# Kernel tuning notes

Measured on AMD Instinct MI355X. Metric: run time of the kernel, lower is better.

## Reference

```python
import jax, jax.numpy as jnp
import numpy as np

B, N, D, H = 32, 2048, 1024, 16
HD = D // H


def setup_inputs() -> dict:
    key = jax.random.key(0)
    ks = jax.random.split(key, 12)
    s = 1.0 / np.sqrt(D)  # xavier-ish scale for square projections
    return {
        "z": jax.random.normal(ks[0], (B, N, D), dtype=jnp.float32),
        "mask": jax.random.bernoulli(ks[1], 0.9, (B, N)),
        "query": jax.random.normal(ks[2], (1, 1, D), dtype=jnp.float32) * s,
        "w_q": jax.random.normal(ks[3], (D, D), dtype=jnp.float32) * s,
        "w_k": jax.random.normal(ks[4], (D, D), dtype=jnp.float32) * s,
        "w_v": jax.random.normal(ks[5], (D, D), dtype=jnp.float32) * s,
        "b_q": jnp.zeros((D,), dtype=jnp.float32),
        "b_k": jnp.zeros((D,), dtype=jnp.float32),
        "b_v": jnp.zeros((D,), dtype=jnp.float32),
        "w_o": jax.random.normal(ks[6], (D, D), dtype=jnp.float32) * s,
        "b_o": jnp.zeros((D,), dtype=jnp.float32),
    }


def reference(z, mask, query, w_q, w_k, w_v, b_q, b_k, b_v, w_o, b_o):
    # mask: True = valid key. Guarantee at least one valid key per row
    # (torch code sets mask[b, 0] = True for all-False rows).
    all_false = ~jnp.any(mask, axis=1)                 # [B]
    valid = mask.at[:, 0].set(mask[:, 0] | all_false)  # [B, N]

    # Projections (PyTorch Linear: x @ W.T + b)
    q = (query @ w_q.T + b_q).reshape(H, HD)           # single shared query -> [H, HD]
    k = (z @ w_k.T + b_k).reshape(B, N, H, HD)
    v = (z @ w_v.T + b_v).reshape(B, N, H, HD)

    scale = 1.0 / jnp.sqrt(jnp.asarray(HD, dtype=z.dtype))
    scores = jnp.einsum('hd,bnhd->bhn', q, k) * scale  # [B, H, N]
    scores = jnp.where(valid[:, None, :], scores, -jnp.inf)
    attn = jax.nn.softmax(scores, axis=-1)             # [B, H, N]

    pooled = jnp.einsum('bhn,bnhd->bhd', attn, v).reshape(B, D)
    return pooled @ w_o.T + b_o                        # [B, D]
```

## Files before the change

kernel.cpp:

```cpp
#include <hip/hip_runtime.h>
#include <hip/hip_bf16.h>
#include <stdint.h>

#define B_ 32
#define N_ 2048
#define D_ 1024
#define H_ 16

#define NT 16
#define RPAD 1028

typedef __attribute__((ext_vector_type(8))) short short8;
typedef __attribute__((ext_vector_type(4))) float f32x4;

__device__ __forceinline__ unsigned short f2bf(float x) {
    unsigned u = __float_as_uint(x);
    u += 0x7FFFu + ((u >> 16) & 1u);
    return (unsigned short)(u >> 16);
}
__device__ __forceinline__ float bflo(unsigned u) { return __uint_as_float(u << 16); }

__device__ __forceinline__ short8 cvt8(float4 a, float4 b) {
    union { __hip_bfloat162 h[4]; short8 s; } u;
    u.h[0] = __float22bfloat162_rn(make_float2(a.x, a.y));
    u.h[1] = __float22bfloat162_rn(make_float2(a.z, a.w));
    u.h[2] = __float22bfloat162_rn(make_float2(b.x, b.y));
    u.h[3] = __float22bfloat162_rn(make_float2(b.z, b.w));
    return u.s;
}

__global__ __launch_bounds__(256) void prep_k(const float* __restrict__ query,
        const float* __restrict__ w_q, const float* __restrict__ b_q,
        const float* __restrict__ w_k, const int* __restrict__ mask,
        unsigned short* __restrict__ rAf, int* __restrict__ any_ws) {
    __shared__ __align__(16) float qv[1024];
    __shared__ float qp[64][5];
    __shared__ float qh[64];
    __shared__ int wf[4];
    int bx = blockIdx.x, t = threadIdx.x;
    if (bx < 64) {
        int h = bx >> 2, dg = bx & 3;
        *(float4*)&qv[4 * t] = *(const float4*)&query[4 * t];
        __syncthreads();
        {
            int j = t >> 2, sub = t & 3;
            const float4* wq4 = (const float4*)(w_q + (size_t)(h * 64 + j) * 1024);
            const float4* qv4 = (const float4*)qv;
            float a = 0.f;
            #pragma unroll 8
            for (int kk = 0; kk < 64; kk++) {
                float4 wv = wq4[sub * 64 + kk];
                float4 vv = qv4[sub * 64 + kk];
                a += wv.x * vv.x + wv.y * vv.y + wv.z * vv.z + wv.w * vv.w;
            }
            qp[j][sub] = a;
        }
        __syncthreads();
        if (t < 64)
            qh[t] = qp[t][0] + qp[t][1] + qp[t][2] + qp[t][3] + b_q[h * 64 + t];
        __syncthreads();
        int d = dg * 256 + t;
        float acc = 0.f;
        #pragma unroll 8
        for (int j = 0; j < 64; j++)
            acc += qh[j] * w_k[(size_t)(h * 64 + j) * 1024 + d];
        acc *= 0.125f;
        int i = d >> 5, fq = (d >> 3) & 3, jj = d & 7;
        int lane = (fq << 4) | h;
        rAf[(size_t)(i * 64 + lane) * 8 + jj] = f2bf(acc);
    } else {
        int b = bx - 64;
        int v = 0;
        for (int k = 0; k < 8; k++) v |= mask[b * N_ + k * 256 + t];
        unsigned long long bal = __ballot(v != 0);
        int w = t >> 6;
        if ((t & 63) == 0) wf[w] = (bal != 0ull) ? 1 : 0;
        __syncthreads();
        if (t == 0) any_ws[b] = wf[0] | wf[1] | wf[2] | wf[3];
    }
}

__global__ __launch_bounds__(512, 2) void main_k(const float* __restrict__ z,
        const int* __restrict__ mask, const int* __restrict__ any_ws,
        const unsigned short* __restrict__ rAf,
        unsigned short* __restrict__ part, float* __restrict__ l_part) {
    __shared__ __align__(16) float zt[2][16 * RPAD];
    __shared__ __align__(16) float Ew[8][16][16];
    __shared__ int mlds[256];
    int bx = blockIdx.x, t = threadIdx.x;
    int b = bx >> 3, c = bx & 7;
    int n0 = c * 256;
    int w = t >> 6, l = t & 63;
    int frow = l & 15, fquad = l >> 4;
    int anyb = any_ws[b];

    short8 rA[32];
    {
        const short8* rA8 = (const short8*)rAf;
        #pragma unroll
        for (int i = 0; i < 32; i++) rA[i] = rA8[i * 64 + l];
    }
    const float* zb = z + (size_t)b * N_ * D_ + (size_t)n0 * D_;

    if (t < 256) mlds[t] = mask[b * N_ + n0 + t];

    float2 ctx[16];
    #pragma unroll
    for (int h = 0; h < 16; h++) ctx[h] = make_float2(0.f, 0.f);
    float l4[4] = {0.f, 0.f, 0.f, 0.f};

    #define STAGE(p, tile)                                                        \
        {                                                                         \
            _Pragma("unroll")                                                     \
            for (int rr = 0; rr < 2; rr++) {                                      \
                int row = 2 * w + rr;                                             \
                const float* gsrc = zb + (size_t)(tile) * 16 * D_ +               \
                                    (size_t)row * D_ + l * 4;                     \
                float* ldst = &zt[(p)][row * RPAD];                               \
                _Pragma("unroll")                                                 \
                for (int q = 0; q < 4; q++) {                                     \
                    __builtin_amdgcn_global_load_lds(                             \
                        (const __attribute__((address_space(1))) unsigned int*)   \
                            (gsrc + q * 256),                                     \
                        (__attribute__((address_space(3))) unsigned int*)         \
                            (ldst + q * 256),                                     \
                        16, 0, 0);                                                \
                }                                                                 \
            }                                                                     \
        }

    STAGE(0, 0)
    __syncthreads();

    for (int it = 0; it < NT; it++) {
        int p = it & 1;
        if (it + 1 < NT) STAGE(p ^ 1, it + 1)

        f32x4 a0 = {0.f,0.f,0.f,0.f}, a1 = {0.f,0.f,0.f,0.f};
        f32x4 a2 = {0.f,0.f,0.f,0.f}, a3 = {0.f,0.f,0.f,0.f};
        const float* brow = &zt[p][frow * RPAD + fquad * 8];
        #pragma unroll
        for (int i = 0; i < 32; i += 4) {
            float4 z00 = *(const float4*)(brow + (i + 0) * 32);
            float4 z01 = *(const float4*)(brow + (i + 0) * 32 + 4);
            float4 z10 = *(const float4*)(brow + (i + 1) * 32);
            float4 z11 = *(const float4*)(brow + (i + 1) * 32 + 4);
            float4 z20 = *(const float4*)(brow + (i + 2) * 32);
            float4 z21 = *(const float4*)(brow + (i + 2) * 32 + 4);
            float4 z30 = *(const float4*)(brow + (i + 3) * 32);
            float4 z31 = *(const float4*)(brow + (i + 3) * 32 + 4);
            a0 = __builtin_amdgcn_mfma_f32_16x16x32_bf16(rA[i + 0], cvt8(z00, z01), a0, 0, 0, 0);
            a1 = __builtin_amdgcn_mfma_f32_16x16x32_bf16(rA[i + 1], cvt8(z10, z11), a1, 0, 0, 0);
            a2 = __builtin_amdgcn_mfma_f32_16x16x32_bf16(rA[i + 2], cvt8(z20, z21), a2, 0, 0, 0);
            a3 = __builtin_amdgcn_mfma_f32_16x16x32_bf16(rA[i + 3], cvt8(z30, z31), a3, 0, 0, 0);
        }
        f32x4 acc = a0 + a1 + a2 + a3;

        {
            int gn = n0 + it * 16 + frow;
            bool valid = (mlds[it * 16 + frow] != 0) || (gn == 0 && anyb == 0);
            float e0 = valid ? __expf(acc[0]) : 0.f;
            float e1 = valid ? __expf(acc[1]) : 0.f;
            float e2 = valid ? __expf(acc[2]) : 0.f;
            float e3 = valid ? __expf(acc[3]) : 0.f;
            l4[0] += e0; l4[1] += e1; l4[2] += e2; l4[3] += e3;
            *(float4*)&Ew[w][frow][fquad * 4] = make_float4(e0, e1, e2, e3);
        }

        {
            const float* zcol = &zt[p][w * 128 + 2 * l];
            #pragma unroll 4
            for (int r = 0; r < 16; r++) {
                float2 zr = *(const float2*)(zcol + r * RPAD);
                const float4* er4 = (const float4*)&Ew[w][r][0];
                float4 e0 = er4[0], e1 = er4[1], e2 = er4[2], e3 = er4[3];
                ctx[0].x  += e0.x * zr.x; ctx[0].y  += e0.x * zr.y;
                ctx[1].x  += e0.y * zr.x; ctx[1].y  += e0.y * zr.y;
                ctx[2].x  += e0.z * zr.x; ctx[2].y  += e0.z * zr.y;
                ctx[3].x  += e0.w * zr.x; ctx[3].y  += e0.w * zr.y;
                ctx[4].x  += e1.x * zr.x; ctx[4].y  += e1.x * zr.y;
                ctx[5].x  += e1.y * zr.x; ctx[5].y  += e1.y * zr.y;
                ctx[6].x  += e1.z * zr.x; ctx[6].y  += e1.z * zr.y;
                ctx[7].x  += e1.w * zr.x; ctx[7].y  += e1.w * zr.y;
                ctx[8].x  += e2.x * zr.x; ctx[8].y  += e2.x * zr.y;
                ctx[9].x  += e2.y * zr.x; ctx[9].y  += e2.y * zr.y;
                ctx[10].x += e2.z * zr.x; ctx[10].y += e2.z * zr.y;
                ctx[11].x += e2.w * zr.x; ctx[11].y += e2.w * zr.y;
                ctx[12].x += e3.x * zr.x; ctx[12].y += e3.x * zr.y;
                ctx[13].x += e3.y * zr.x; ctx[13].y += e3.y * zr.y;
                ctx[14].x += e3.z * zr.x; ctx[14].y += e3.z * zr.y;
                ctx[15].x += e3.w * zr.x; ctx[15].y += e3.w * zr.y;
            }
        }
        __syncthreads();
    }

    {
        unsigned short* pp = part + (size_t)bx * 16 * 1024 + w * 128 + 2 * l;
        #pragma unroll
        for (int h = 0; h < 16; h++) {
            ushort2 o;
            o.x = f2bf(ctx[h].x); o.y = f2bf(ctx[h].y);
            *(ushort2*)(pp + h * 1024) = o;
        }
    }
    if (w == 0) {
        #pragma unroll
        for (int r = 0; r < 4; r++) {
            float v = l4[r];
            v += __shfl_xor(v, 1, 64);
            v += __shfl_xor(v, 2, 64);
            v += __shfl_xor(v, 4, 64);
            v += __shfl_xor(v, 8, 64);
            if (frow == 0) l_part[bx * 16 + fquad * 4 + r] = v;
        }
    }
}

__global__ __launch_bounds__(256) void gemv_wv_k(const unsigned short* __restrict__ part,
        const float* __restrict__ l_part, const float* __restrict__ w_v,
        const float* __restrict__ b_v, float* __restrict__ pooled) {
    __shared__ __align__(16) float vlds[1024];
    int bx = blockIdx.x, t = threadIdx.x;
    int b = bx >> 4, h = bx & 15;
    float L = 0.f;
    #pragma unroll
    for (int cc = 0; cc < 8; cc++) L += l_part[(b * 8 + cc) * 16 + h];
    float rL = 1.f / L;
    float sx = 0.f, sy = 0.f, sz = 0.f, sw = 0.f;
    #pragma unroll
    for (int cc = 0; cc < 8; cc++) {
        const ushort4* p4 = (const ushort4*)&part[(((size_t)(b * 8 + cc)) * 16 + h) * 1024];
        ushort4 u = p4[t];
        sx += bflo(u.x); sy += bflo(u.y); sz += bflo(u.z); sw += bflo(u.w);
    }
    *(float4*)&vlds[4 * t] = make_float4(sx * rL, sy * rL, sz * rL, sw * rL);
    __syncthreads();
    int w = t >> 6, l = t & 63;
    const float4* v4 = (const float4*)vlds;
    float* orow = pooled + (size_t)b * 1024;
    #pragma unroll
    for (int s0 = 0; s0 < 16; s0 += 4) {
        int jb = h * 64 + w * 16 + s0;
        float a0 = 0.f, a1 = 0.f, a2 = 0.f, a3 = 0.f;
        #pragma unroll
        for (int kk = 0; kk < 4; kk++) {
            float4 v = v4[kk * 64 + l];
            float4 w0 = *(const float4*)&w_v[(size_t)(jb + 0) * 1024 + (kk * 64 + l) * 4];
            float4 w1 = *(const float4*)&w_v[(size_t)(jb + 1) * 1024 + (kk * 64 + l) * 4];
            float4 w2 = *(const float4*)&w_v[(size_t)(jb + 2) * 1024 + (kk * 64 + l) * 4];
            float4 w3 = *(const float4*)&w_v[(size_t)(jb + 3) * 1024 + (kk * 64 + l) * 4];
            a0 += w0.x * v.x + w0.y * v.y + w0.z * v.z + w0.w * v.w;
            a1 += w1.x * v.x + w1.y * v.y + w1.z * v.z + w1.w * v.w;
            a2 += w2.x * v.x + w2.y * v.y + w2.z * v.z + w2.w * v.w;
            a3 += w3.x * v.x + w3.y * v.y + w3.z * v.z + w3.w * v.w;
        }
        #pragma unroll
        for (int m = 32; m >= 1; m >>= 1) {
            a0 += __shfl_xor(a0, m, 64); a1 += __shfl_xor(a1, m, 64);
            a2 += __shfl_xor(a2, m, 64); a3 += __shfl_xor(a3, m, 64);
        }
        if (l == 0) {
            orow[jb + 0] = a0 + b_v[jb + 0];
            orow[jb + 1] = a1 + b_v[jb + 1];
            orow[jb + 2] = a2 + b_v[jb + 2];
            orow[jb + 3] = a3 + b_v[jb + 3];
        }
    }
}

__global__ __launch_bounds__(256) void gemv_wo_k(const float* __restrict__ pooled,
        const float* __restrict__ w_o, const float* __restrict__ b_o,
        float* __restrict__ out) {
    __shared__ __align__(16) float vlds[1024];
    int bx = blockIdx.x, t = threadIdx.x;
    int b = bx >> 4, q = bx & 15;
    *(float4*)&vlds[4 * t] = *(const float4*)&pooled[(size_t)b * 1024 + 4 * t];
    __syncthreads();
    int w = t >> 6, l = t & 63;
    const float4* v4 = (const float4*)vlds;
    float* orow = out + (size_t)b * 1024;
    #pragma unroll
    for (int s0 = 0; s0 < 16; s0 += 4) {
        int jb = q * 64 + w * 16 + s0;
        float a0 = 0.f, a1 = 0.f, a2 = 0.f, a3 = 0.f;
        #pragma unroll
        for (int kk = 0; kk < 4; kk++) {
            float4 v = v4[kk * 64 + l];
            float4 w0 = *(const float4*)&w_o[(size_t)(jb + 0) * 1024 + (kk * 64 + l) * 4];
            float4 w1 = *(const float4*)&w_o[(size_t)(jb + 1) * 1024 + (kk * 64 + l) * 4];
            float4 w2 = *(const float4*)&w_o[(size_t)(jb + 2) * 1024 + (kk * 64 + l) * 4];
            float4 w3 = *(const float4*)&w_o[(size_t)(jb + 3) * 1024 + (kk * 64 + l) * 4];
            a0 += w0.x * v.x + w0.y * v.y + w0.z * v.z + w0.w * v.w;
            a1 += w1.x * v.x + w1.y * v.y + w1.z * v.z + w1.w * v.w;
            a2 += w2.x * v.x + w2.y * v.y + w2.z * v.z + w2.w * v.w;
            a3 += w3.x * v.x + w3.y * v.y + w3.z * v.z + w3.w * v.w;
        }
        #pragma unroll
        for (int m = 32; m >= 1; m >>= 1) {
            a0 += __shfl_xor(a0, m, 64); a1 += __shfl_xor(a1, m, 64);
            a2 += __shfl_xor(a2, m, 64); a3 += __shfl_xor(a3, m, 64);
        }
        if (l == 0) {
            orow[jb + 0] = a0 + b_o[jb + 0];
            orow[jb + 1] = a1 + b_o[jb + 1];
            orow[jb + 2] = a2 + b_o[jb + 2];
            orow[jb + 3] = a3 + b_o[jb + 3];
        }
    }
}

extern "C" void kernel_launch(void* const* d_in, const int* in_sizes, int n_in,
                              void* d_out, int out_size, void* d_ws, size_t ws_size,
                              hipStream_t stream) {
    const float* z     = (const float*)d_in[0];
    const int*   mask  = (const int*)d_in[1];
    const float* query = (const float*)d_in[2];
    const float* w_q   = (const float*)d_in[3];
    const float* w_k   = (const float*)d_in[4];
    const float* w_v   = (const float*)d_in[5];
    const float* b_q   = (const float*)d_in[6];
    const float* b_v   = (const float*)d_in[8];
    const float* w_o   = (const float*)d_in[9];
    const float* b_o   = (const float*)d_in[10];
    float* out = (float*)d_out;

    char* ws = (char*)d_ws;
    unsigned short* rAf    = (unsigned short*)(ws + 0);
    int*            any_ws = (int*)(ws + 32768);
    float*          l_part = (float*)(ws + 40960);
    float*          pooled = (float*)(ws + 65536);
    unsigned short* part   = (unsigned short*)(ws + 1048576);

    prep_k<<<96, 256, 0, stream>>>(query, w_q, b_q, w_k, mask, rAf, any_ws);
    main_k<<<256, 512, 0, stream>>>(z, mask, any_ws, rAf, part, l_part);
    gemv_wv_k<<<512, 256, 0, stream>>>(part, l_part, w_v, b_v, pooled);
    gemv_wo_k<<<512, 256, 0, stream>>>(pooled, w_o, b_o, out);
}
```

Measured before the change: 494.4 us.

## Split score MFMA across warps with LDS reduction instead of redundant per-warp compute

Previously every warp computed the full 1024-wide score dot product redundantly, holding all 32 bf16 A fragments in registers. Now each warp computes a 128-wide slice with 4 MFMAs, partial scores are reduced through shared memory, and exp/mask is done once by 256 threads into a shared E tile. This cuts redundant MFMA work and LDS reads and frees registers. In exchange it adds two extra block barriers per tile and moves the next-tile prefetch later, which may reduce overlap. Launch bounds drop to 1 block per CU.

Result: faster. 423.6 us (-14.3%).

```diff
diff --git a/kernel.cpp b/kernel.cpp
--- a/kernel.cpp
+++ b/kernel.cpp
@@ -80,12 +80,14 @@
     }
 }
 
-__global__ __launch_bounds__(512, 2) void main_k(const float* __restrict__ z,
+__global__ __launch_bounds__(512, 1) void main_k(const float* __restrict__ z,
         const int* __restrict__ mask, const int* __restrict__ any_ws,
         const unsigned short* __restrict__ rAf,
         unsigned short* __restrict__ part, float* __restrict__ l_part) {
     __shared__ __align__(16) float zt[2][16 * RPAD];
-    __shared__ __align__(16) float Ew[8][16][16];
+    __shared__ __align__(16) float Sp[8][16][16];
+    __shared__ __align__(16) float E[16][16];
+    __shared__ float Lr[4][16];
     __shared__ int mlds[256];
     int bx = blockIdx.x, t = threadIdx.x;
     int b = bx >> 3, c = bx & 7;
@@ -94,11 +96,11 @@
     int frow = l & 15, fquad = l >> 4;
     int anyb = any_ws[b];
 
-    short8 rA[32];
+    short8 rA[4];
     {
         const short8* rA8 = (const short8*)rAf;
         #pragma unroll
-        for (int i = 0; i < 32; i++) rA[i] = rA8[i * 64 + l];
+        for (int i = 0; i < 4; i++) rA[i] = rA8[(4 * w + i) * 64 + l];
     }
     const float* zb = z + (size_t)b * N_ * D_ + (size_t)n0 * D_;
 
@@ -107,7 +109,7 @@
     float2 ctx[16];
     #pragma unroll
     for (int h = 0; h < 16; h++) ctx[h] = make_float2(0.f, 0.f);
-    float l4[4] = {0.f, 0.f, 0.f, 0.f};
+    float lacc = 0.f;
 
     #define STAGE(p, tile)                                                        \
         {                                                                         \
@@ -134,45 +136,48 @@
 
     for (int it = 0; it < NT; it++) {
         int p = it & 1;
+
+        {
+            f32x4 a0 = {0.f, 0.f, 0.f, 0.f}, a1 = {0.f, 0.f, 0.f, 0.f};
+            const float* brow = &zt[p][frow * RPAD + w * 128 + fquad * 8];
+            float4 z00 = *(const float4*)(brow + 0 * 32);
+            float4 z01 = *(const float4*)(brow + 0 * 32 + 4);
+            float4 z10 = *(const float4*)(brow + 1 * 32);
+            float4 z11 = *(const float4*)(brow + 1 * 32 + 4);
+            float4 z20 = *(const float4*)(brow + 2 * 32);
+            float4 z21 = *(const float4*)(brow + 2 * 32 + 4);
+            float4 z30 = *(const float4*)(brow + 3 * 32);
+            float4 z31 = *(const float4*)(brow + 3 * 32 + 4);
+            a0 = __builtin_amdgcn_mfma_f32_16x16x32_bf16(rA[0], cvt8(z00, z01), a0, 0, 0, 0);
+            a1 = __builtin_amdgcn_mfma_f32_16x16x32_bf16(rA[1], cvt8(z10, z11), a1, 0, 0, 0);
+            a0 = __builtin_amdgcn_mfma_f32_16x16x32_bf16(rA[2], cvt8(z20, z21), a0, 0, 0, 0);
+            a1 = __builtin_amdgcn_mfma_f32_16x16x32_bf16(rA[3], cvt8(z30, z31), a1, 0, 0, 0);
+            f32x4 acc = a0 + a1;
+            *(f32x4*)&Sp[w][frow][fquad * 4] = acc;
+        }
+        __syncthreads();
+
+        if (t < 256) {
+            const float* sp = &Sp[0][0][0];
+            float s = sp[t] + sp[256 + t] + sp[512 + t] + sp[768 + t] +
+                      sp[1024 + t] + sp[1280 + t] + sp[1536 + t] + sp[1792 + t];
+            int n = t >> 4;
+            int gn = n0 + it * 16 + n;
+            bool valid = (mlds[it * 16 + n] != 0) || (gn == 0 && anyb == 0);
+            float ev = valid ? __expf(s) : 0.f;
+            lacc += ev;
+            ((float*)E)[t] = ev;
+        }
+        __syncthreads();
+
         if (it + 1 < NT) STAGE(p ^ 1, it + 1)
-
-        f32x4 a0 = {0.f,0.f,0.f,0.f}, a1 = {0.f,0.f,0.f,0.f};
-        f32x4 a2 = {0.f,0.f,0.f,0.f}, a3 = {0.f,0.f,0.f,0.f};
-        const float* brow = &zt[p][frow * RPAD + fquad * 8];
-        #pragma unroll
-        for (int i = 0; i < 32; i += 4) {
-            float4 z00 = *(const float4*)(brow + (i + 0) * 32);
-            float4 z01 = *(const float4*)(brow + (i + 0) * 32 + 4);
-            float4 z10 = *(const float4*)(brow + (i + 1) * 32);
-            float4 z11 = *(const float4*)(brow + (i + 1) * 32 + 4);
-            float4 z20 = *(const float4*)(brow + (i + 2) * 32);
-            float4 z21 = *(const float4*)(brow + (i + 2) * 32 + 4);
-            float4 z30 = *(const float4*)(brow + (i + 3) * 32);
-            float4 z31 = *(const float4*)(brow + (i + 3) * 32 + 4);
-            a0 = __builtin_amdgcn_mfma_f32_16x16x32_bf16(rA[i + 0], cvt8(z00, z01), a0, 0, 0, 0);
-            a1 = __builtin_amdgcn_mfma_f32_16x16x32_bf16(rA[i + 1], cvt8(z10, z11), a1, 0, 0, 0);
-            a2 = __builtin_amdgcn_mfma_f32_16x16x32_bf16(rA[i + 2], cvt8(z20, z21), a2, 0, 0, 0);
-            a3 = __builtin_amdgcn_mfma_f32_16x16x32_bf16(rA[i + 3], cvt8(z30, z31), a3, 0, 0, 0);
-        }
-        f32x4 acc = a0 + a1 + a2 + a3;
-
-        {
-            int gn = n0 + it * 16 + frow;
-            bool valid = (mlds[it * 16 + frow] != 0) || (gn == 0 && anyb == 0);
-            float e0 = valid ? __expf(acc[0]) : 0.f;
-            float e1 = valid ? __expf(acc[1]) : 0.f;
-            float e2 = valid ? __expf(acc[2]) : 0.f;
-            float e3 = valid ? __expf(acc[3]) : 0.f;
-            l4[0] += e0; l4[1] += e1; l4[2] += e2; l4[3] += e3;
-            *(float4*)&Ew[w][frow][fquad * 4] = make_float4(e0, e1, e2, e3);
-        }
 
         {
             const float* zcol = &zt[p][w * 128 + 2 * l];
             #pragma unroll 4
             for (int r = 0; r < 16; r++) {
                 float2 zr = *(const float2*)(zcol + r * RPAD);
-                const float4* er4 = (const float4*)&Ew[w][r][0];
+                const float4* er4 = (const float4*)&E[r][0];
                 float4 e0 = er4[0], e1 = er4[1], e2 = er4[2], e3 = er4[3];
                 ctx[0].x  += e0.x * zr.x; ctx[0].y  += e0.x * zr.y;
                 ctx[1].x  += e0.y * zr.x; ctx[1].y  += e0.y * zr.y;
@@ -204,17 +209,14 @@
             *(ushort2*)(pp + h * 1024) = o;
         }
     }
-    if (w == 0) {
-        #pragma unroll
-        for (int r = 0; r < 4; r++) {
-            float v = l4[r];
-            v += __shfl_xor(v, 1, 64);
-            v += __shfl_xor(v, 2, 64);
-            v += __shfl_xor(v, 4, 64);
-            v += __shfl_xor(v, 8, 64);
-            if (frow == 0) l_part[bx * 16 + fquad * 4 + r] = v;
-        }
-    }
+    if (t < 256) {
+        float v = lacc;
+        v += __shfl_xor(v, 16, 64);
+        v += __shfl_xor(v, 32, 64);
+        if (l < 16) Lr[w][l] = v;
+    }
+    __syncthreads();
+    if (t < 16) l_part[bx * 16 + t] = Lr[0][t] + Lr[1][t] + Lr[2][t] + Lr[3][t];
 }
 
 __global__ __launch_bounds__(256) void gemv_wv_k(const unsigned short* __restrict__ part,
```
